# Optimization experiments

Hardware: AMD Instinct MI355X
Metric: run time of the kernel (lower is better)

The kernel has to match this reference:

```python
import jax, jax.numpy as jnp
import numpy as np

D_MODEL = 1024
NUM_HEADS = 16
D_K = D_MODEL // NUM_HEADS
NEG_INF = -1e9


def setup_inputs() -> dict:
    key = jax.random.key(0)
    ks = jax.random.split(key, 12)
    B, S = 2, 2048
    scale = 1.0 / np.sqrt(D_MODEL)
    inp = {
        "q": jax.random.normal(ks[0], (B, S, D_MODEL), jnp.float32),
        "k": jax.random.normal(ks[1], (B, S, D_MODEL), jnp.float32),
        "v": jax.random.normal(ks[2], (B, S, D_MODEL), jnp.float32),
        "mask": jnp.ones((B, S), jnp.int32),
        "W_q": jax.random.normal(ks[3], (D_MODEL, D_MODEL), jnp.float32) * scale,
        "b_q": jnp.zeros((D_MODEL,), jnp.float32),
        "W_k": jax.random.normal(ks[4], (D_MODEL, D_MODEL), jnp.float32) * scale,
        "b_k": jnp.zeros((D_MODEL,), jnp.float32),
        "W_v": jax.random.normal(ks[5], (D_MODEL, D_MODEL), jnp.float32) * scale,
        "b_v": jnp.zeros((D_MODEL,), jnp.float32),
        "W_o": jax.random.normal(ks[6], (D_MODEL, D_MODEL), jnp.float32) * scale,
        "b_o": jnp.zeros((D_MODEL,), jnp.float32),
    }
    return inp


def reference(q, k, v, mask, W_q, b_q, W_k, b_k, W_v, b_v, W_o, b_o):
    B, S, _ = q.shape
    def proj(x, W, b):
        # [B,S,D] -> [B,H,S,d_k]
        y = x @ W.T + b
        return y.reshape(B, -1, NUM_HEADS, D_K).transpose(0, 2, 1, 3)
    qh = proj(q, W_q, b_q)
    kh = proj(k, W_k, b_k)
    vh = proj(v, W_v, b_v)
    scores = jnp.einsum("bhqd,bhkd->bhqk", qh, kh) / jnp.sqrt(jnp.float32(D_K))
    # 2D mask [B,S_k] -> broadcast over heads and query positions
    m = mask[:, None, None, :]
    scores = jnp.where(m == 0, jnp.float32(NEG_INF), scores)
    attn = jax.nn.softmax(scores, axis=-1)
    # dropout is identity at inference
    context = jnp.einsum("bhqk,bhkd->bhqd", attn, vh)
    context = context.transpose(0, 2, 1, 3).reshape(B, S, D_MODEL)
    return context @ W_o.T + b_o
```

## Files before the change

kernel.cpp:

```cpp
#include <hip/hip_runtime.h>
#include <hip/hip_bf16.h>
#include <cstdint>
#include <cstddef>

#define DMODEL 1024
#define NHEADS 16
#define DK 64
#define SEQ 2048
#define BATCH 2
#define NT2 (SEQ / 64)

typedef short bf16x8 __attribute__((ext_vector_type(8)));
typedef float f32x4 __attribute__((ext_vector_type(4)));
typedef float f32x16 __attribute__((ext_vector_type(16)));
typedef unsigned int u32x2 __attribute__((ext_vector_type(2)));
typedef unsigned int u32x4 __attribute__((ext_vector_type(4)));

typedef const __attribute__((address_space(1))) void* gas_ptr;
typedef __attribute__((address_space(3))) void* las_ptr;

__device__ __forceinline__ void gld_lds16(const void* g, void* l) {
    __builtin_amdgcn_global_load_lds((gas_ptr)g, (las_ptr)l, 16, 0, 0);
}

__device__ __forceinline__ ushort f2bf_u(float f) {
    uint32_t x = __float_as_uint(f);
    x += 0x7fff + ((x >> 16) & 1);
    return (ushort)(x >> 16);
}

__global__ __launch_bounds__(256) void cast_all(
        const float* __restrict__ q, const float* __restrict__ k,
        const float* __restrict__ v, const float* __restrict__ Wq,
        const float* __restrict__ Wk, const float* __restrict__ Wv,
        const float* __restrict__ Wo,
        ushort* __restrict__ qb, ushort* __restrict__ kb, ushort* __restrict__ vb,
        ushort* __restrict__ Wqb, ushort* __restrict__ Wkb,
        ushort* __restrict__ Wvb, ushort* __restrict__ Wob) {
    int bid = blockIdx.x;
    const float* src; ushort* dst; int base;
    if      (bid <  4096) { src = q;  dst = qb;  base = bid; }
    else if (bid <  8192) { src = k;  dst = kb;  base = bid - 4096; }
    else if (bid < 12288) { src = v;  dst = vb;  base = bid - 8192; }
    else if (bid < 13312) { src = Wq; dst = Wqb; base = bid - 12288; }
    else if (bid < 14336) { src = Wk; dst = Wkb; base = bid - 13312; }
    else if (bid < 15360) { src = Wv; dst = Wvb; base = bid - 14336; }
    else                  { src = Wo; dst = Wob; base = bid - 15360; }
    int i = base * 1024 + threadIdx.x * 4;
    float4 f = *reinterpret_cast<const float4*>(src + i);
    ushort4 o;
    o.x = f2bf_u(f.x); o.y = f2bf_u(f.y); o.z = f2bf_u(f.z); o.w = f2bf_u(f.w);
    *reinterpret_cast<ushort4*>(dst + i) = o;
}

__global__ __launch_bounds__(256) void mask2bias(
        const int* __restrict__ m, float* __restrict__ mb) {
    int i = (blockIdx.x * 256 + threadIdx.x) * 4;
    int4 mk = *reinterpret_cast<const int4*>(m + i);
    float4 o;
    o.x = mk.x ? 0.f : -1e9f;
    o.y = mk.y ? 0.f : -1e9f;
    o.z = mk.z ? 0.f : -1e9f;
    o.w = mk.w ? 0.f : -1e9f;
    *reinterpret_cast<float4*>(mb + i) = o;
}

__global__ __launch_bounds__(256) void gemm_qkv(
        const ushort* __restrict__ A,
        const ushort* __restrict__ Wall,
        const float* __restrict__ bq, const float* __restrict__ bk,
        const float* __restrict__ bv,
        ushort* __restrict__ Qh, ushort* __restrict__ Kh, ushort* __restrict__ Vt) {
    __shared__ ushort As[128 * 32];
    __shared__ ushort Bs[128 * 32];
    const int tid = threadIdx.x;
    const int w = tid >> 6, lane = tid & 63;
    const int lr = lane & 15, lg = lane >> 4;
    int lid = (blockIdx.x & 7) * 96 + (blockIdx.x >> 3);
    const int tMg = (lid >> 3) << 7;
    const int tN  = (lid & 7) << 7;
    const int g   = tMg >> 12;
    const ushort* W = Wall + (size_t)g * 1024 * 1024;
    const float* bias = (g == 0) ? bq : (g == 1 ? bk : bv);
    const int wr = (w >> 1) * 64, wc = (w & 1) * 64;

    f32x4 acc[4][4] = {};

    const int c0 = (w * 2 + 0) * 64 + lane;
    const int c1 = (w * 2 + 1) * 64 + lane;
    const ushort* gA0 = A + (size_t)(tMg + (c0 >> 2)) * 1024 + (c0 & 3) * 8;
    const ushort* gA1 = A + (size_t)(tMg + (c1 >> 2)) * 1024 + (c1 & 3) * 8;
    const ushort* gB0 = W + (size_t)(tN + (c0 >> 2)) * 1024 + (c0 & 3) * 8;
    const ushort* gB1 = W + (size_t)(tN + (c1 >> 2)) * 1024 + (c1 & 3) * 8;
    ushort* lA0 = As + (w * 2 + 0) * 512;
    ushort* lA1 = As + (w * 2 + 1) * 512;
    ushort* lB0 = Bs + (w * 2 + 0) * 512;
    ushort* lB1 = Bs + (w * 2 + 1) * 512;

    for (int k0 = 0; k0 < 1024; k0 += 32) {
        gld_lds16(gA0 + k0, lA0);
        gld_lds16(gA1 + k0, lA1);
        gld_lds16(gB0 + k0, lB0);
        gld_lds16(gB1 + k0, lB1);
        __syncthreads();

        bf16x8 af[4], bfr[4];
#pragma unroll
        for (int i = 0; i < 4; i++)
            af[i] = *(const bf16x8*)(As + (wr + i * 16 + lr) * 32 + lg * 8);
#pragma unroll
        for (int i = 0; i < 4; i++)
            bfr[i] = *(const bf16x8*)(Bs + (wc + i * 16 + lr) * 32 + lg * 8);
#pragma unroll
        for (int mi = 0; mi < 4; mi++)
#pragma unroll
            for (int ni = 0; ni < 4; ni++)
                acc[mi][ni] = __builtin_amdgcn_mfma_f32_16x16x32_bf16(
                    af[mi], bfr[ni], acc[mi][ni], 0, 0, 0);
        __syncthreads();
    }

#pragma unroll
    for (int mi = 0; mi < 4; mi++) {
        const int row0 = tMg + wr + mi * 16 + lg * 4;
#pragma unroll
        for (int ni = 0; ni < 4; ni++) {
            const int col = tN + wc + ni * 16 + lr;
            const int h = col >> 6, d = col & (DK - 1);
            const float bvv = bias[col];
#pragma unroll
            for (int r = 0; r < 4; r++) {
                float vv = acc[mi][ni][r] + bvv;
                int mloc = (row0 + r) & 4095;
                int b = mloc >> 11, s = mloc & (SEQ - 1);
                if (g == 0)
                    Qh[(((size_t)(b * NHEADS + h) * SEQ + s) * DK) + d] = f2bf_u(vv);
                else if (g == 1)
                    Kh[(((size_t)(b * NHEADS + h) * SEQ + s) * DK) + d] = f2bf_u(vv);
                else
                    Vt[(((size_t)(b * NHEADS + h) * DK + d) * SEQ) + s] = f2bf_u(vv);
            }
        }
    }
}

__global__ __launch_bounds__(256) void gemm_out(
        const ushort* __restrict__ A,
        const ushort* __restrict__ W,
        const float* __restrict__ bias,
        float* __restrict__ out, int M, int N, int K) {
    __shared__ ushort As[64 * 32];
    __shared__ ushort Bs[128 * 32];
    const int tid = threadIdx.x;
    const int w = tid >> 6, lane = tid & 63;
    const int lr = lane & 15, lg = lane >> 4;
    const int nTiles = N >> 7;
    const int cpx = gridDim.x >> 3;
    int lid = (blockIdx.x & 7) * cpx + (blockIdx.x >> 3);
    const int tM = (lid / nTiles) << 6;
    const int tN = (lid % nTiles) << 7;
    const int wr = (w >> 1) * 32, wc = (w & 1) * 64;

    f32x4 acc[2][4] = {};

    const int cA = w * 64 + lane;
    const int cB0 = w * 128 + lane;
    const int cB1 = w * 128 + 64 + lane;
    const ushort* gA  = A + (size_t)(tM + (cA  >> 2)) * K + (cA  & 3) * 8;
    const ushort* gB0 = W + (size_t)(tN + (cB0 >> 2)) * K + (cB0 & 3) * 8;
    const ushort* gB1 = W + (size_t)(tN + (cB1 >> 2)) * K + (cB1 & 3) * 8;
    ushort* lA  = As + w * 512;
    ushort* lB0 = Bs + w * 1024;
    ushort* lB1 = Bs + w * 1024 + 512;

    for (int k0 = 0; k0 < K; k0 += 32) {
        gld_lds16(gA  + k0, lA);
        gld_lds16(gB0 + k0, lB0);
        gld_lds16(gB1 + k0, lB1);
        __syncthreads();

        bf16x8 af[2], bfr[4];
#pragma unroll
        for (int i = 0; i < 2; i++)
            af[i] = *(const bf16x8*)(As + (wr + i * 16 + lr) * 32 + lg * 8);
#pragma unroll
        for (int i = 0; i < 4; i++)
            bfr[i] = *(const bf16x8*)(Bs + (wc + i * 16 + lr) * 32 + lg * 8);
#pragma unroll
        for (int mi = 0; mi < 2; mi++)
#pragma unroll
            for (int ni = 0; ni < 4; ni++)
                acc[mi][ni] = __builtin_amdgcn_mfma_f32_16x16x32_bf16(
                    af[mi], bfr[ni], acc[mi][ni], 0, 0, 0);
        __syncthreads();
    }

#pragma unroll
    for (int mi = 0; mi < 2; mi++) {
        const int row0 = tM + wr + mi * 16 + lg * 4;
#pragma unroll
        for (int ni = 0; ni < 4; ni++) {
            const int col = tN + wc + ni * 16 + lr;
            const float bv = bias[col];
#pragma unroll
            for (int r = 0; r < 4; r++)
                out[(size_t)(row0 + r) * N + col] = acc[mi][ni][r] + bv;
        }
    }
}

#define SCALE2 0.18033688011120542f

__device__ __forceinline__ bf16x8 pack_pa(const float* p) {
    uint a, b, c, d;
    asm("v_cvt_pk_bf16_f32 %0, %1, %2" : "=v"(a) : "v"(p[0]), "v"(p[1]));
    asm("v_cvt_pk_bf16_f32 %0, %1, %2" : "=v"(b) : "v"(p[4]), "v"(p[5]));
    asm("v_cvt_pk_bf16_f32 %0, %1, %2" : "=v"(c) : "v"(p[2]), "v"(p[3]));
    asm("v_cvt_pk_bf16_f32 %0, %1, %2" : "=v"(d) : "v"(p[6]), "v"(p[7]));
    asm("v_permlane32_swap_b32 %0, %1" : "+v"(a), "+v"(b));
    asm("v_permlane32_swap_b32 %0, %1" : "+v"(c), "+v"(d));
    union { u32x4 u; bf16x8 h; } cv;
    cv.u = (u32x4){a, c, b, d};
    return cv.h;
}

__device__ __forceinline__ float xmax32(float x) {
    u32x2 r = __builtin_amdgcn_permlane32_swap(__float_as_uint(x), __float_as_uint(x), false, false);
    return fmaxf(__uint_as_float(r[0]), __uint_as_float(r[1]));
}
__device__ __forceinline__ float xadd32(float x) {
    u32x2 r = __builtin_amdgcn_permlane32_swap(__float_as_uint(x), __float_as_uint(x), false, false);
    return __uint_as_float(r[0]) + __uint_as_float(r[1]);
}

__global__ __launch_bounds__(256) void attn_fwd32(
        const ushort* __restrict__ Qh, const ushort* __restrict__ Kh,
        const ushort* __restrict__ Vt, const float* __restrict__ mbias,
        ushort* __restrict__ ctx) {
    __shared__ ushort Ks[2][2][2048];
    __shared__ ushort Vs[2][2][2048];
    __shared__ float  Ml[SEQ];

    const int tid = threadIdx.x;
    const int w = tid >> 6;
    const int l = tid & 63;
    const int q32 = l & 31, hi = l >> 5;
    const int q7 = l & 7;

    int lid = (blockIdx.x & 7) * 64 + (blockIdx.x >> 3);
    const int qblk = lid & 15;
    const int bh = lid >> 4;
    const int b = bh >> 4;
    const int h = bh & 15;
    const int q0 = qblk * 128 + w * 32;

    const ushort* Qp = Qh + (size_t)bh * SEQ * DK + (size_t)(q0 + q32) * DK + hi * 8;
    const ushort* Kg = Kh + (size_t)bh * SEQ * DK;
    const ushort* Vg = Vt + (size_t)bh * DK * SEQ;

    const int srow = tid >> 3;
    const int scs  = (tid & 7) ^ (srow & 7);
    const ushort* Ksrc = Kg + (size_t)srow * DK + scs * 8;
    const ushort* Vsrc = Vg + (size_t)(srow + ((scs & 4) << 3)) * SEQ + (scs & 3) * 8;

    {
        const float* mg = mbias + (size_t)b * SEQ;
        gld_lds16(mg + tid * 4,        &Ml[w * 256]);
        gld_lds16(mg + 1024 + tid * 4, &Ml[1024 + w * 256]);
    }

    auto STAGE = [&](int buf, int t) {
        const int kv0 = t * 64;
        gld_lds16(Ksrc + (size_t)kv0 * DK,        &Ks[buf][0][w * 512]);
        gld_lds16(Ksrc + (size_t)(kv0 + 32) * DK, &Ks[buf][1][w * 512]);
        gld_lds16(Vsrc + kv0,                     &Vs[buf][0][w * 512]);
        gld_lds16(Vsrc + kv0 + 32,                &Vs[buf][1][w * 512]);
    };

    bf16x8 qf[4];
#pragma unroll
    for (int dc = 0; dc < 4; dc++)
        qf[dc] = *(const bf16x8*)(Qp + dc * 16);

    f32x16 c0 = {}, c1 = {};
    float m2 = -1e30f, lrun = 0.f;

    STAGE(0, 0);
    __syncthreads();

    for (int t = 0; t < NT2; ++t) {
        const int buf = t & 1;
        if (t + 1 < NT2) STAGE(buf ^ 1, t + 1);

        const int kv0 = t * 64;

        bf16x8 kf0[4], kf1[4];
#pragma unroll
        for (int dc = 0; dc < 4; dc++)
            kf0[dc] = *(const bf16x8*)(&Ks[buf][0][q32 * 64 + (((dc * 2 + hi) ^ q7) * 8)]);
#pragma unroll
        for (int dc = 0; dc < 4; dc++)
            kf1[dc] = *(const bf16x8*)(&Ks[buf][1][q32 * 64 + (((dc * 2 + hi) ^ q7) * 8)]);
        f32x16 s0 = {}, s1 = {};
        __builtin_amdgcn_s_setprio(1);
#pragma unroll
        for (int dc = 0; dc < 4; dc++) {
            s0 = __builtin_amdgcn_mfma_f32_32x32x16_bf16(kf0[dc], qf[dc], s0, 0, 0, 0);
            s1 = __builtin_amdgcn_mfma_f32_32x32x16_bf16(kf1[dc], qf[dc], s1, 0, 0, 0);
        }
        __builtin_amdgcn_s_setprio(0);

        float p0[16], p1[16];
#pragma unroll
        for (int g = 0; g < 4; g++) {
            float4 mb0 = *reinterpret_cast<const float4*>(&Ml[kv0 + g * 8 + hi * 4]);
            float4 mb1 = *reinterpret_cast<const float4*>(&Ml[kv0 + 32 + g * 8 + hi * 4]);
#pragma unroll
            for (int j = 0; j < 4; j++) {
                p0[g * 4 + j] = fmaf(s0[g * 4 + j], SCALE2, reinterpret_cast<const float*>(&mb0)[j]);
                p1[g * 4 + j] = fmaf(s1[g * 4 + j], SCALE2, reinterpret_cast<const float*>(&mb1)[j]);
            }
        }

        float pm = fmaxf(p0[0], p1[0]);
#pragma unroll
        for (int r = 1; r < 16; r++) pm = fmaxf(pm, fmaxf(p0[r], p1[r]));
        pm = xmax32(pm);
        if (__any(pm - m2 > 8.0f)) {
            float mnew = fmaxf(m2, pm);
            float alpha = __builtin_amdgcn_exp2f(m2 - mnew);
            m2 = mnew; lrun *= alpha;
#pragma unroll
            for (int r = 0; r < 16; r++) {
                float aT = __shfl(alpha, (r & 3) + 8 * (r >> 2) + 4 * hi);
                c0[r] *= aT; c1[r] *= aT;
            }
        }

        float rs = 0.f;
#pragma unroll
        for (int r = 0; r < 16; r++) {
            p0[r] = __builtin_amdgcn_exp2f(p0[r] - m2);
            p1[r] = __builtin_amdgcn_exp2f(p1[r] - m2);
            rs += p0[r] + p1[r];
        }
        lrun += rs;

        bf16x8 pa00 = pack_pa(p0);
        bf16x8 pa01 = pack_pa(p0 + 8);
        bf16x8 pa10 = pack_pa(p1);
        bf16x8 pa11 = pack_pa(p1 + 8);

        bf16x8 vc0[4], vc1[4];
#pragma unroll
        for (int dt = 0; dt < 2; dt++)
#pragma unroll
            for (int ks = 0; ks < 2; ks++) {
                vc0[dt * 2 + ks] = *(const bf16x8*)(&Vs[buf][0][q32 * 64 + (((dt * 4 + ks * 2 + hi) ^ q7) * 8)]);
                vc1[dt * 2 + ks] = *(const bf16x8*)(&Vs[buf][1][q32 * 64 + (((dt * 4 + ks * 2 + hi) ^ q7) * 8)]);
            }

        __builtin_amdgcn_s_setprio(1);
        c0 = __builtin_amdgcn_mfma_f32_32x32x16_bf16(pa00, vc0[0], c0, 0, 0, 0);
        c1 = __builtin_amdgcn_mfma_f32_32x32x16_bf16(pa00, vc0[2], c1, 0, 0, 0);
        c0 = __builtin_amdgcn_mfma_f32_32x32x16_bf16(pa01, vc0[1], c0, 0, 0, 0);
        c1 = __builtin_amdgcn_mfma_f32_32x32x16_bf16(pa01, vc0[3], c1, 0, 0, 0);
        c0 = __builtin_amdgcn_mfma_f32_32x32x16_bf16(pa10, vc1[0], c0, 0, 0, 0);
        c1 = __builtin_amdgcn_mfma_f32_32x32x16_bf16(pa10, vc1[2], c1, 0, 0, 0);
        c0 = __builtin_amdgcn_mfma_f32_32x32x16_bf16(pa11, vc1[1], c0, 0, 0, 0);
        c1 = __builtin_amdgcn_mfma_f32_32x32x16_bf16(pa11, vc1[3], c1, 0, 0, 0);
        __builtin_amdgcn_s_setprio(0);

        __syncthreads();
    }

    float rl = 1.0f / xadd32(lrun);
#pragma unroll
    for (int r = 0; r < 16; r++) {
        int crow = (r & 3) + 8 * (r >> 2) + 4 * hi;
        float rlT = __shfl(rl, crow);
        int qq = q0 + crow;
        size_t base = (size_t)(b * SEQ + qq) * DMODEL + h * DK;
        ctx[base + q32]      = f2bf_u(c0[r] * rlT);
        ctx[base + 32 + q32] = f2bf_u(c1[r] * rlT);
    }
}

extern "C" void kernel_launch(void* const* d_in, const int* in_sizes, int n_in,
                              void* d_out, int out_size, void* d_ws, size_t ws_size,
                              hipStream_t stream) {
    const float* q    = (const float*)d_in[0];
    const float* k    = (const float*)d_in[1];
    const float* v    = (const float*)d_in[2];
    const int*   mask = (const int*)d_in[3];
    const float* Wq   = (const float*)d_in[4];
    const float* bq   = (const float*)d_in[5];
    const float* Wk   = (const float*)d_in[6];
    const float* bk   = (const float*)d_in[7];
    const float* Wv   = (const float*)d_in[8];
    const float* bv   = (const float*)d_in[9];
    const float* Wo   = (const float*)d_in[10];
    const float* bo   = (const float*)d_in[11];

    char* ws = (char*)d_ws;
    ushort* qb   = (ushort*)(ws + (size_t)0);
    ushort* kb   = (ushort*)(ws + ((size_t)8  << 20));
    ushort* vb   = (ushort*)(ws + ((size_t)16 << 20));
    ushort* Wqb  = (ushort*)(ws + ((size_t)24 << 20));
    ushort* Wkb  = (ushort*)(ws + ((size_t)26 << 20));
    ushort* Wvb  = (ushort*)(ws + ((size_t)28 << 20));
    ushort* Wob  = (ushort*)(ws + ((size_t)30 << 20));
    ushort* Qh   = (ushort*)(ws + ((size_t)32 << 20));
    ushort* Kh   = (ushort*)(ws + ((size_t)40 << 20));
    ushort* Vt   = (ushort*)(ws + ((size_t)48 << 20));
    ushort* ctxb = (ushort*)(ws + ((size_t)56 << 20));
    float*  mbias = (float*)(ws + (size_t)0);

    cast_all<<<16384, 256, 0, stream>>>(q, k, v, Wq, Wk, Wv, Wo,
                                        qb, kb, vb, Wqb, Wkb, Wvb, Wob);

    gemm_qkv<<<768, 256, 0, stream>>>(qb, Wqb, bq, bk, bv, Qh, Kh, Vt);

    mask2bias<<<BATCH * SEQ / 1024, 256, 0, stream>>>(mask, mbias);

    attn_fwd32<<<BATCH * NHEADS * (SEQ / 128), 256, 0, stream>>>(Qh, Kh, Vt, mbias, ctxb);

    const int M = BATCH * SEQ;
    gemm_out<<<(M / 64) * (DMODEL / 128), 256, 0, stream>>>(
        ctxb, Wob, bo, (float*)d_out, M, DMODEL, DMODEL);
}
```

Before: 147.5 us.

## Split attention tile into two 32-key halves with separate online-softmax steps

Each 64-key tile is now processed as two 32-key sub-tiles. Each half gets its own score MFMA, max, rescale check, exp and PV MFMA, so one half's softmax work can interleave with the other half's MFMAs. Tree reductions replace the serial max and sum chains. The cost is a possible second rescale per tile and two extra cross-lane max reductions, and the compiler may schedule the code no better than before.

After: 146.6 us. About the same (-0.6%).

```diff
diff --git a/kernel.cpp b/kernel.cpp
--- a/kernel.cpp
+++ b/kernel.cpp
@@ -233,6 +233,24 @@
     return __uint_as_float(r[0]) + __uint_as_float(r[1]);
 }
 
+__device__ __forceinline__ float tmax16(const float* p) {
+    float a0 = fmaxf(p[0], p[1]),   a1 = fmaxf(p[2], p[3]);
+    float a2 = fmaxf(p[4], p[5]),   a3 = fmaxf(p[6], p[7]);
+    float a4 = fmaxf(p[8], p[9]),   a5 = fmaxf(p[10], p[11]);
+    float a6 = fmaxf(p[12], p[13]), a7 = fmaxf(p[14], p[15]);
+    float b0 = fmaxf(a0, a1), b1 = fmaxf(a2, a3);
+    float b2 = fmaxf(a4, a5), b3 = fmaxf(a6, a7);
+    return fmaxf(fmaxf(b0, b1), fmaxf(b2, b3));
+}
+__device__ __forceinline__ float tsum16(const float* p) {
+    float a0 = p[0] + p[1],   a1 = p[2] + p[3];
+    float a2 = p[4] + p[5],   a3 = p[6] + p[7];
+    float a4 = p[8] + p[9],   a5 = p[10] + p[11];
+    float a6 = p[12] + p[13], a7 = p[14] + p[15];
+    float b0 = a0 + a1, b1 = a2 + a3, b2 = a4 + a5, b3 = a6 + a7;
+    return (b0 + b1) + (b2 + b3);
+}
+
 __global__ __launch_bounds__(256) void attn_fwd32(
         const ushort* __restrict__ Qh, const ushort* __restrict__ Kh,
         const ushort* __restrict__ Vt, const float* __restrict__ mbias,
@@ -298,36 +316,33 @@
 #pragma unroll
         for (int dc = 0; dc < 4; dc++)
             kf0[dc] = *(const bf16x8*)(&Ks[buf][0][q32 * 64 + (((dc * 2 + hi) ^ q7) * 8)]);
+        f32x16 s0 = {}, s1 = {};
+        __builtin_amdgcn_s_setprio(1);
+#pragma unroll
+        for (int dc = 0; dc < 4; dc++)
+            s0 = __builtin_amdgcn_mfma_f32_32x32x16_bf16(kf0[dc], qf[dc], s0, 0, 0, 0);
+        __builtin_amdgcn_s_setprio(0);
 #pragma unroll
         for (int dc = 0; dc < 4; dc++)
             kf1[dc] = *(const bf16x8*)(&Ks[buf][1][q32 * 64 + (((dc * 2 + hi) ^ q7) * 8)]);
-        f32x16 s0 = {}, s1 = {};
         __builtin_amdgcn_s_setprio(1);
 #pragma unroll
-        for (int dc = 0; dc < 4; dc++) {
-            s0 = __builtin_amdgcn_mfma_f32_32x32x16_bf16(kf0[dc], qf[dc], s0, 0, 0, 0);
+        for (int dc = 0; dc < 4; dc++)
             s1 = __builtin_amdgcn_mfma_f32_32x32x16_bf16(kf1[dc], qf[dc], s1, 0, 0, 0);
-        }
         __builtin_amdgcn_s_setprio(0);
 
-        float p0[16], p1[16];
+        float p0[16];
 #pragma unroll
         for (int g = 0; g < 4; g++) {
             float4 mb0 = *reinterpret_cast<const float4*>(&Ml[kv0 + g * 8 + hi * 4]);
-            float4 mb1 = *reinterpret_cast<const float4*>(&Ml[kv0 + 32 + g * 8 + hi * 4]);
-#pragma unroll
-            for (int j = 0; j < 4; j++) {
-                p0[g * 4 + j] = fmaf(s0[g * 4 + j], SCALE2, reinterpret_cast<const float*>(&mb0)[j]);
-                p1[g * 4 + j] = fmaf(s1[g * 4 + j], SCALE2, reinterpret_cast<const float*>(&mb1)[j]);
-            }
-        }
-
-        float pm = fmaxf(p0[0], p1[0]);
-#pragma unroll
-        for (int r = 1; r < 16; r++) pm = fmaxf(pm, fmaxf(p0[r], p1[r]));
-        pm = xmax32(pm);
-        if (__any(pm - m2 > 8.0f)) {
-            float mnew = fmaxf(m2, pm);
+#pragma unroll
+            for (int j = 0; j < 4; j++)
+                p0[g * 4 + j] = fmaf(s0[g * 4 + j], SCALE2,
+                                     reinterpret_cast<const float*>(&mb0)[j]);
+        }
+        float pm0 = xmax32(tmax16(p0));
+        if (__any(pm0 - m2 > 8.0f)) {
+            float mnew = fmaxf(m2, pm0);
             float alpha = __builtin_amdgcn_exp2f(m2 - mnew);
             m2 = mnew; lrun *= alpha;
 #pragma unroll
@@ -336,40 +351,65 @@
                 c0[r] *= aT; c1[r] *= aT;
             }
         }
-
-        float rs = 0.f;
-#pragma unroll
-        for (int r = 0; r < 16; r++) {
-            p0[r] = __builtin_amdgcn_exp2f(p0[r] - m2);
-            p1[r] = __builtin_amdgcn_exp2f(p1[r] - m2);
-            rs += p0[r] + p1[r];
-        }
-        lrun += rs;
-
-        bf16x8 pa00 = pack_pa(p0);
-        bf16x8 pa01 = pack_pa(p0 + 8);
-        bf16x8 pa10 = pack_pa(p1);
-        bf16x8 pa11 = pack_pa(p1 + 8);
-
-        bf16x8 vc0[4], vc1[4];
+        float e0[16];
+#pragma unroll
+        for (int r = 0; r < 16; r++)
+            e0[r] = __builtin_amdgcn_exp2f(p0[r] - m2);
+        bf16x8 pa00 = pack_pa(e0);
+        bf16x8 pa01 = pack_pa(e0 + 8);
+        bf16x8 vc0[4];
 #pragma unroll
         for (int dt = 0; dt < 2; dt++)
 #pragma unroll
-            for (int ks = 0; ks < 2; ks++) {
+            for (int ks = 0; ks < 2; ks++)
                 vc0[dt * 2 + ks] = *(const bf16x8*)(&Vs[buf][0][q32 * 64 + (((dt * 4 + ks * 2 + hi) ^ q7) * 8)]);
-                vc1[dt * 2 + ks] = *(const bf16x8*)(&Vs[buf][1][q32 * 64 + (((dt * 4 + ks * 2 + hi) ^ q7) * 8)]);
-            }
-
         __builtin_amdgcn_s_setprio(1);
         c0 = __builtin_amdgcn_mfma_f32_32x32x16_bf16(pa00, vc0[0], c0, 0, 0, 0);
         c1 = __builtin_amdgcn_mfma_f32_32x32x16_bf16(pa00, vc0[2], c1, 0, 0, 0);
         c0 = __builtin_amdgcn_mfma_f32_32x32x16_bf16(pa01, vc0[1], c0, 0, 0, 0);
         c1 = __builtin_amdgcn_mfma_f32_32x32x16_bf16(pa01, vc0[3], c1, 0, 0, 0);
+        __builtin_amdgcn_s_setprio(0);
+        lrun += tsum16(e0);
+
+        float p1[16];
+#pragma unroll
+        for (int g = 0; g < 4; g++) {
+            float4 mb1 = *reinterpret_cast<const float4*>(&Ml[kv0 + 32 + g * 8 + hi * 4]);
+#pragma unroll
+            for (int j = 0; j < 4; j++)
+                p1[g * 4 + j] = fmaf(s1[g * 4 + j], SCALE2,
+                                     reinterpret_cast<const float*>(&mb1)[j]);
+        }
+        float pm1 = xmax32(tmax16(p1));
+        if (__any(pm1 - m2 > 8.0f)) {
+            float mnew = fmaxf(m2, pm1);
+            float alpha = __builtin_amdgcn_exp2f(m2 - mnew);
+            m2 = mnew; lrun *= alpha;
+#pragma unroll
+            for (int r = 0; r < 16; r++) {
+                float aT = __shfl(alpha, (r & 3) + 8 * (r >> 2) + 4 * hi);
+                c0[r] *= aT; c1[r] *= aT;
+            }
+        }
+        float e1[16];
+#pragma unroll
+        for (int r = 0; r < 16; r++)
+            e1[r] = __builtin_amdgcn_exp2f(p1[r] - m2);
+        bf16x8 pa10 = pack_pa(e1);
+        bf16x8 pa11 = pack_pa(e1 + 8);
+        bf16x8 vc1[4];
+#pragma unroll
+        for (int dt = 0; dt < 2; dt++)
+#pragma unroll
+            for (int ks = 0; ks < 2; ks++)
+                vc1[dt * 2 + ks] = *(const bf16x8*)(&Vs[buf][1][q32 * 64 + (((dt * 4 + ks * 2 + hi) ^ q7) * 8)]);
+        __builtin_amdgcn_s_setprio(1);
         c0 = __builtin_amdgcn_mfma_f32_32x32x16_bf16(pa10, vc1[0], c0, 0, 0, 0);
         c1 = __builtin_amdgcn_mfma_f32_32x32x16_bf16(pa10, vc1[2], c1, 0, 0, 0);
         c0 = __builtin_amdgcn_mfma_f32_32x32x16_bf16(pa11, vc1[1], c0, 0, 0, 0);
         c1 = __builtin_amdgcn_mfma_f32_32x32x16_bf16(pa11, vc1[3], c1, 0, 0, 0);
         __builtin_amdgcn_s_setprio(0);
+        lrun += tsum16(e1);
 
         __syncthreads();
     }
```
